# Performance work log

Hardware: AMD Instinct MI355X
Metric: run time of the kernel (lower is better)

The kernel has to match this reference:

```python
import jax, jax.numpy as jnp
import numpy as np
from jax.scipy.special import logsumexp

B, K = 256, 6144            # batch, info block length (n = 3K, rate 1/3)
NUM_ITER = 6
MU = 3                      # memory of RSC code (constraint_length 4)
NS = 1 << MU                # 8 trellis states
G0 = (1, 0, 1, 1)           # feedback polynomial '1011'
G1 = (1, 1, 0, 1)           # output polynomial  '1101'
NEG = -1e30


def _build_trellis():
    nxt = np.zeros((NS, 2), np.int32)
    par = np.zeros((NS, 2), np.int32)
    for s in range(NS):
        r = [(s >> (MU - 1 - j)) & 1 for j in range(MU)]  # r[0] newest register bit
        for u in (0, 1):
            fb = (u + sum(G0[j + 1] * r[j] for j in range(MU))) % 2
            p = (G1[0] * fb + sum(G1[j + 1] * r[j] for j in range(MU))) % 2
            nxt[s, u] = (fb << (MU - 1)) | (s >> 1)
            par[s, u] = p
    prev_s = np.zeros((NS, 2), np.int32)
    prev_u = np.zeros((NS, 2), np.int32)
    cnt = np.zeros(NS, np.int32)
    for s in range(NS):
        for u in (0, 1):
            sn = nxt[s, u]
            prev_s[sn, cnt[sn]] = s
            prev_u[sn, cnt[sn]] = u
            cnt[sn] += 1
    return nxt, par, prev_s, prev_u

_NXT, _PAR, _PREV_S, _PREV_U = _build_trellis()


def bcjr(l_sys, l_par, l_a):
    """log-MAP BCJR on the rate-1/2 RSC trellis. LLR convention log p(0)/p(1).
    l_sys, l_par, l_a: [B, K] -> posterior LLR [B, K]."""
    nxt = jnp.asarray(_NXT)
    prev_s = jnp.asarray(_PREV_S)
    prev_u = jnp.asarray(_PREV_U)
    par_sign = jnp.asarray(1.0 - 2.0 * _PAR, l_sys.dtype)  # [NS,2]
    u_sign = jnp.asarray([1.0, -1.0], l_sys.dtype)         # (1-2u)
    b = l_sys.shape[0]
    lsu = (l_sys + l_a).T                                  # [K,B]
    lp = l_par.T
    # branch metrics gamma[t, b, s, u] = 0.5*((1-2u)(Lsys+La) + (1-2p)Lpar)
    gamma = 0.5 * (lsu[:, :, None, None] * u_sign + lp[:, :, None, None] * par_sign)
    alpha0 = jnp.full((b, NS), NEG, l_sys.dtype).at[:, 0].set(0.0)  # start in state 0

    def fwd(alpha, g):
        a = logsumexp(alpha[:, prev_s] + g[:, prev_s, prev_u], axis=-1)  # [B,NS]
        a = a - jnp.max(a, axis=-1, keepdims=True)
        return a, alpha

    _, alphas = jax.lax.scan(fwd, alpha0, gamma)           # alphas[t] = alpha_t  [K,B,NS]
    beta_end = jnp.zeros((b, NS), l_sys.dtype)             # unterminated: uniform

    def bwd(beta, g):
        bn = logsumexp(g + beta[:, nxt], axis=-1)          # [B,NS]
        bn = bn - jnp.max(bn, axis=-1, keepdims=True)
        return bn, beta

    _, betas1 = jax.lax.scan(bwd, beta_end, gamma, reverse=True)  # betas1[t] = beta_{t+1}
    m = alphas[..., None] + gamma + betas1[:, :, nxt]      # [K,B,NS,2]
    l_post = logsumexp(m[..., 0], axis=-1) - logsumexp(m[..., 1], axis=-1)  # [K,B]
    return l_post.T


def turbo_decode(inputs, perm):
    llr = -inputs                 # sionna logits log p1/p0 -> internal LLR log p0/p1
    ls1 = llr[:, 0::3]            # systematic
    lp1 = llr[:, 1::3]            # parity of encoder 1
    lp2 = llr[:, 2::3]            # parity of encoder 2
    ls2 = ls1[:, perm]            # interleaved systematic for decoder 2
    inv = jnp.argsort(perm)       # deinterleave index
    le2_de = jnp.zeros_like(ls1)
    for _ in range(NUM_ITER):
        la1 = le2_de
        lpost1 = bcjr(ls1, lp1, la1)
        le1 = lpost1 - la1 - ls1                  # extrinsic of decoder 1
        la2 = le1[:, perm]
        lpost2 = bcjr(ls2, lp2, la2)
        le2_de = (lpost2 - la2 - ls2)[:, inv]     # deinterleaved extrinsic of decoder 2
    return -lpost2[:, inv]        # soft output, back to logit convention (hard_out=False)


def setup_inputs() -> dict:
    key = jax.random.key(0)
    k1, k2 = jax.random.split(key)
    inputs = jax.random.normal(k1, (B, 3 * K), dtype=jnp.float32)
    perm = jax.random.permutation(k2, K)
    return {"inputs": inputs, "perm": perm}


def reference(inputs, perm):
    return turbo_decode(inputs, perm)
```

## Files before the change

kernel.cpp:

```cpp
#include <hip/hip_runtime.h>
#include <hip/hip_fp16.h>

constexpr int B_ = 256;
constexpr int K_ = 6144;
constexpr int NITER = 6;
constexpr int L_ = 6;
constexpr int W0_ = 6;
constexpr int C_ = K_ / L_;
constexpr float LOG2E = 1.4426950408889634f;
constexpr float LN2   = 0.6931471805599453f;

static_assert(K_ % L_ == 0, "");
static_assert((L_ % 2) == 0 && (W0_ % 2) == 0, "");
static_assert(W0_ <= L_, "uniform-warmup trick requires W0 <= L");

#if __has_builtin(__builtin_amdgcn_exp2f)
#define EXP2F(x) __builtin_amdgcn_exp2f(x)
#else
#define EXP2F(x) exp2f(x)
#endif
#if __has_builtin(__builtin_amdgcn_logf)
#define LOG2F(x) __builtin_amdgcn_logf(x)
#else
#define LOG2F(x) log2f(x)
#endif
#if __has_builtin(__builtin_amdgcn_rcpf)
#define RCPF(x) __builtin_amdgcn_rcpf(x)
#else
#define RCPF(x) (1.0f / (x))
#endif

__device__ __forceinline__ float b2f(unsigned short u) {
  return __uint_as_float((unsigned)u << 16);
}
__device__ __forceinline__ unsigned short f2b(float f) {
  unsigned u = __float_as_uint(f);
  u += 0x7FFFu + ((u >> 16) & 1u);
  return (unsigned short)(u >> 16);
}
__device__ __forceinline__ float h2f_bits(unsigned short us) {
  __half_raw r; r.x = us; return __half2float(__half(r));
}
__device__ __forceinline__ unsigned short f2h_bits(float f) {
  return __half_as_ushort(__float2half(f));
}

__device__ __forceinline__ unsigned int ld_dev_u32(const unsigned int* p) {
  return __hip_atomic_load(const_cast<unsigned int*>(p), __ATOMIC_RELAXED,
                           __HIP_MEMORY_SCOPE_AGENT);
}
__device__ __forceinline__ void st_dev_u32(unsigned int* p, unsigned int v) {
  __hip_atomic_store(p, v, __ATOMIC_RELAXED, __HIP_MEMORY_SCOPE_AGENT);
}
__device__ __forceinline__ unsigned long long ld_dev_u64(
    const unsigned long long* p) {
  return __hip_atomic_load(const_cast<unsigned long long*>(p),
                           __ATOMIC_RELAXED, __HIP_MEMORY_SCOPE_AGENT);
}
__device__ __forceinline__ void st_dev_u64(unsigned long long* p,
                                           unsigned long long v) {
  __hip_atomic_store(p, v, __ATOMIC_RELAXED, __HIP_MEMORY_SCOPE_AGENT);
}

__device__ __forceinline__ void gam_lin(float gxv, float gyv, float g[4]) {
  float es = EXP2F(-fabsf(gxv));
  float ep = EXP2F(-fabsf(gyv));
  float fu0 = gxv >= 0.0f ? 1.0f : es;
  float fu1 = gxv >= 0.0f ? es : 1.0f;
  float fp0 = gyv >= 0.0f ? 1.0f : ep;
  float fp1 = gyv >= 0.0f ? ep : 1.0f;
  g[0] = fu0 * fp0; g[1] = fu0 * fp1;
  g[2] = fu1 * fp0; g[3] = fu1 * fp1;
}

__device__ __forceinline__ void step_fwd_lin(float a[8], const float g[4]) {
  float an[8];
#pragma unroll
  for (int sn = 0; sn < 8; ++sn) {
    const int u0 = ((sn >> 2) ^ (sn & 1)) & 1;
    const int p0 = ((sn >> 2) ^ ((sn >> 1) & 1)) & 1;
    an[sn] = a[(sn & 3) * 2] * g[u0 * 2 + p0]
           + a[(sn & 3) * 2 + 1] * g[(u0 ^ 1) * 2 + (p0 ^ 1)];
  }
#pragma unroll
  for (int s = 0; s < 8; ++s) a[s] = an[s];
}

__device__ __forceinline__ void step_bwd_lin(float bt[8], const float g[4]) {
  float bn[8];
#pragma unroll
  for (int s = 0; s < 8; ++s) {
    const int s0 = s & 1, s1b = (s >> 1) & 1, s2b = (s >> 2) & 1;
    const int f0 = s1b ^ s0, q = s1b ^ s2b;
    bn[s] = g[q] * bt[(f0 << 2) | (s >> 1)]
          + g[2 + (q ^ 1)] * bt[((f0 ^ 1) << 2) | (s >> 1)];
  }
#pragma unroll
  for (int s = 0; s < 8; ++s) bt[s] = bn[s];
}

__device__ __forceinline__ void renorm_lin(float a[8]) {
  float m = fmaxf(fmaxf(fmaxf(a[0], a[1]), fmaxf(a[2], a[3])),
                  fmaxf(fmaxf(a[4], a[5]), fmaxf(a[6], a[7])));
  float r = RCPF(fmaxf(m, 1e-30f));
#pragma unroll
  for (int s = 0; s < 8; ++s) a[s] = fmaf(a[s], r, 1e-32f);
}

__device__ __forceinline__ unsigned long long pack8_log8(const float a[8]) {
  unsigned int us[8];
#pragma unroll
  for (int s = 0; s < 8; ++s) {
    float l = -16.0f * LOG2F(a[s]);
    l = fminf(l, 255.0f);
    us[s] = (unsigned int)(l + 0.5f);
  }
  unsigned int x = us[0] | (us[1] << 8) | (us[2] << 16) | (us[3] << 24);
  unsigned int y = us[4] | (us[5] << 8) | (us[6] << 16) | (us[7] << 24);
  return ((unsigned long long)y << 32) | x;
}

__device__ __forceinline__ void unpack8_log8(unsigned long long v, float a[8]) {
  unsigned int vx = (unsigned int)v, vy = (unsigned int)(v >> 32);
#pragma unroll
  for (int s = 0; s < 4; ++s)
    a[s] = EXP2F(-0.0625f * (float)((vx >> (8 * s)) & 0xFFu));
#pragma unroll
  for (int s = 0; s < 4; ++s)
    a[4 + s] = EXP2F(-0.0625f * (float)((vy >> (8 * s)) & 0xFFu));
}

constexpr int NSLOT = 2 * NITER - 1;
constexpr int SLOT_U = 65 * 32;
constexpr int BARS_U = 24576;

__device__ __forceinline__ void tree_barrier(unsigned int* slotBase,
                                             unsigned int gsz) {
  __syncthreads();
  if (threadIdx.x == 0) {
    asm volatile("s_waitcnt vmcnt(0)" ::: "memory");
    const unsigned int g = blockIdx.x & 31u;
    unsigned int* cnt = slotBase + g * 32;
    unsigned int* rel = slotBase + (32 + g) * 32;
    unsigned int* root = slotBase + 64 * 32;
    unsigned int m = __hip_atomic_fetch_add(cnt, 1u, __ATOMIC_RELAXED,
                                            __HIP_MEMORY_SCOPE_AGENT);
    if (m == gsz - 1u) {
      unsigned int r = __hip_atomic_fetch_add(root, 1u, __ATOMIC_RELAXED,
                                              __HIP_MEMORY_SCOPE_AGENT);
      if (r == 31u) {
#pragma unroll
        for (int gg = 0; gg < 32; ++gg)
          st_dev_u32(slotBase + (32 + gg) * 32, 1u);
      }
    }
    while (!ld_dev_u32(rel))
      __builtin_amdgcn_s_sleep(2);
  }
  __syncthreads();
}

struct WSL {
  float* lpostT;
  __half* gx1; __half* gx2;
  unsigned short* gy1; unsigned short* gy2;
  __half* ls1; __half* ls2;
  int* inv;
  unsigned int* bars;
  unsigned long long *S1a, *S1b, *T1a, *T1b, *S2a, *S2b, *T2a, *T2b;
};

__host__ __device__ inline WSL ws_layout(char* ws) {
  const size_t KB = (size_t)K_ * B_;
  WSL w; char* p = ws;
  w.lpostT = (float*)p;            p += KB * 4;
  w.gx1    = (__half*)p;           p += KB * 2;
  w.gx2    = (__half*)p;           p += KB * 2;
  w.gy1    = (unsigned short*)p;   p += KB * 2;
  w.gy2    = (unsigned short*)p;   p += KB * 2;
  w.ls1    = (__half*)p;           p += KB * 2;
  w.ls2    = (__half*)p;           p += KB * 2;
  w.inv    = (int*)p;              p += (size_t)K_ * 4;
  w.bars   = (unsigned int*)p;     p += (size_t)BARS_U * 4;
  const size_t SB = (size_t)(C_ + 1) * B_;
  w.S1a = (unsigned long long*)p;  p += SB * 8;
  w.S1b = (unsigned long long*)p;  p += SB * 8;
  w.T1a = (unsigned long long*)p;  p += SB * 8;
  w.T1b = (unsigned long long*)p;  p += SB * 8;
  w.S2a = (unsigned long long*)p;  p += SB * 8;
  w.S2b = (unsigned long long*)p;  p += SB * 8;
  w.T2a = (unsigned long long*)p;  p += SB * 8;
  w.T2b = (unsigned long long*)p;  p += SB * 8;
  return w;
}

template <bool DEV>
__device__ __forceinline__ void half_body(
    const int c,
    const __half* __restrict__ gx,
    const unsigned short* __restrict__ gy,
    const __half* __restrict__ lsloc,
    const int* __restrict__ map,
    __half* __restrict__ gxother,
    float* __restrict__ lpost_out,
    const unsigned long long* __restrict__ Sread,
    unsigned long long* __restrict__ Swrite,
    const unsigned long long* __restrict__ Tread,
    unsigned long long* __restrict__ Twrite,
    int wmode, int mode, int wrS, bool gxc) {
  const int b = threadIdx.x;
  const int kv = c * L_;
  const int kend = kv + L_;
  const unsigned int* gxp = (const unsigned int*)gx;
  const int bh = b >> 1;
  const unsigned int hsel = (b & 1) * 16;
  const bool gdev = DEV && !gxc;

  float gvx[L_];
  unsigned short rgy[L_];
  __half hls[L_];
#pragma unroll
  for (int i = 0; i < L_; ++i) {
    size_t o2 = (size_t)(kv + i) * (B_ / 2) + bh;
    unsigned int u = gdev ? ld_dev_u32(gxp + o2) : gxp[o2];
    gvx[i] = h2f_bits((unsigned short)(u >> hsel));
    rgy[i] = gy[(size_t)(kv + i) * B_ + b];
  }
  if (mode == 0) {
#pragma unroll
    for (int i = 0; i < L_; ++i)
      hls[i] = lsloc[(size_t)(kv + i) * B_ + b];
  }
  int jmap[L_];
#pragma unroll
  for (int i = 0; i < L_; ++i) jmap[i] = map[kv + i];
  unsigned long long sraw = 0, traw = 0;
  float wfx[W0_], wbx[W0_];
  unsigned short wfy[W0_], wby[W0_];
  if (wmode == 2) {
    if (c > 0) {
      const size_t o = (size_t)c * B_ + b;
      sraw = DEV ? ld_dev_u64(Sread + o) : Sread[o];
    }
    if (c < C_ - 1) {
      const size_t o = (size_t)(c + 1) * B_ + b;
      traw = DEV ? ld_dev_u64(Tread + o) : Tread[o];
    }
  } else {
    if (c > 0) {
#pragma unroll
      for (int q = 0; q < W0_; ++q) {
        size_t o2 = (size_t)(kv - W0_ + q) * (B_ / 2) + bh;
        unsigned int u = gdev ? ld_dev_u32(gxp + o2) : gxp[o2];
        wfx[q] = h2f_bits((unsigned short)(u >> hsel));
        wfy[q] = gy[(size_t)(kv - W0_ + q) * B_ + b];
      }
    }
    if (c < C_ - 1) {
#pragma unroll
      for (int q = 0; q < W0_; ++q) {
        size_t o2 = (size_t)(kend + W0_ - 1 - q) * (B_ / 2) + bh;
        unsigned int u = gdev ? ld_dev_u32(gxp + o2) : gxp[o2];
        wbx[q] = h2f_bits((unsigned short)(u >> hsel));
        wby[q] = gy[(size_t)(kend + W0_ - 1 - q) * B_ + b];
      }
    }
  }

  float gc[L_][4];
#pragma unroll
  for (int i = 0; i < L_; ++i) gam_lin(gvx[i], b2f(rgy[i]), gc[i]);

  float a[8];
  if (c == 0) {
    a[0] = 1.0f;
#pragma unroll
    for (int s = 1; s < 8; ++s) a[s] = 0.0f;
  } else if (wmode == 0) {
    if (c == 1) {
      a[0] = 1.0f;
#pragma unroll
      for (int s = 1; s < 8; ++s) a[s] = 0.0f;
    } else {
#pragma unroll
      for (int s = 0; s < 8; ++s) a[s] = 1.0f;
    }
#pragma unroll
    for (int q = 0; q < W0_; ++q) {
      float g[4];
      gam_lin(wfx[q], b2f(wfy[q]), g);
      step_fwd_lin(a, g);
      if (q & 1) renorm_lin(a);
    }
  } else {
    unpack8_log8(sraw, a);
  }
  float a2d[L_][8];
#pragma unroll
  for (int i = 0; i < L_; ++i) {
#pragma unroll
    for (int s = 0; s < 8; ++s) a2d[i][s] = a[s];
    step_fwd_lin(a, gc[i]);
    if (i & 1) renorm_lin(a);
  }
  if (wrS) {
    unsigned long long v = pack8_log8(a);
    unsigned long long* p = Swrite + (size_t)(c + 1) * B_ + b;
    if (DEV) st_dev_u64(p, v); else *p = v;
  }

  float bt[8];
  if (c == C_ - 1) {
#pragma unroll
    for (int s = 0; s < 8; ++s) bt[s] = 1.0f;
  } else if (wmode == 0) {
#pragma unroll
    for (int s = 0; s < 8; ++s) bt[s] = 1.0f;
#pragma unroll
    for (int q = 0; q < W0_; ++q) {
      float g[4];
      gam_lin(wbx[q], b2f(wby[q]), g);
      step_bwd_lin(bt, g);
      if (q & 1) renorm_lin(bt);
    }
  } else {
    unpack8_log8(traw, bt);
  }
#pragma unroll
  for (int ii = 0; ii < L_; ++ii) {
    const int i = L_ - 1 - ii;
    const float* g = gc[i];
    float s00 = 0.0f, s01 = 0.0f, s10 = 0.0f, s11 = 0.0f;
    float bn[8];
#pragma unroll
    for (int s = 0; s < 8; ++s) {
      const int s0 = s & 1, s1b = (s >> 1) & 1, s2b = (s >> 2) & 1;
      const int f0 = s1b ^ s0, q = s1b ^ s2b;
      float b0 = bt[(f0 << 2) | (s >> 1)];
      float b1 = bt[((f0 ^ 1) << 2) | (s >> 1)];
      float m0 = a2d[i][s] * b0;
      float m1 = a2d[i][s] * b1;
      if (q == 0) { s00 += m0; s10 += m1; } else { s01 += m0; s11 += m1; }
      bn[s] = g[q] * b0 + g[2 + (q ^ 1)] * b1;
    }
    float t0 = g[0] * s00 + g[1] * s01;
    float t1 = g[3] * s10 + g[2] * s11;
    float lpost = LOG2F(fmaxf(t0, 1e-37f)) - LOG2F(fmaxf(t1, 1e-37f));
    if (mode == 0) {
      float le = lpost - gvx[i];
      unsigned short us = f2h_bits(__half2float(hls[i]) + le);
      unsigned int po = (unsigned int)__shfl_xor((int)us, 1);
      if (!(b & 1)) {
        unsigned int u = (unsigned int)us | (po << 16);
        unsigned int* p =
            (unsigned int*)gxother + ((size_t)jmap[i] * (B_ / 2) + bh);
        if (DEV) st_dev_u32(p, u); else *p = u;
      }
    } else {
      lpost_out[(size_t)jmap[i] * B_ + b] = -LN2 * lpost;
    }
#pragma unroll
    for (int s = 0; s < 8; ++s) bt[s] = bn[s];
    if (ii & 1) renorm_lin(bt);
  }
  if (wrS) {
    unsigned long long v = pack8_log8(bt);
    unsigned long long* p = Twrite + (size_t)c * B_ + b;
    if (DEV) st_dev_u64(p, v); else *p = v;
  }
}

__global__ __launch_bounds__(256, 4) void k_fused(const int* __restrict__ perm,
                                                  char* __restrict__ ws) {
  WSL w = ws_layout(ws);
  const int tid = threadIdx.x;
  const unsigned int gsz = gridDim.x >> 5;

  for (int c = blockIdx.x; c < C_; c += gridDim.x) {
#pragma unroll
    for (int r = 0; r < L_; ++r) {
      const int j = c * L_ + r;
      w.ls2[(size_t)j * B_ + tid] = w.ls1[(size_t)perm[j] * B_ + tid];
    }
  }

  int slot = 0;
  for (int it = 0; it < NITER; ++it) {
    const int pr = it & 1;
    const int wm = (it == 0) ? 0 : 2;
    const int wrS = (it != NITER - 1) ? 1 : 0;
    unsigned long long* S1r = pr ? w.S1b : w.S1a;
    unsigned long long* S1w = pr ? w.S1a : w.S1b;
    unsigned long long* T1r = pr ? w.T1b : w.T1a;
    unsigned long long* T1w = pr ? w.T1a : w.T1b;
    unsigned long long* S2r = pr ? w.S2b : w.S2a;
    unsigned long long* S2w = pr ? w.S2a : w.S2b;
    unsigned long long* T2r = pr ? w.T2b : w.T2a;
    unsigned long long* T2w = pr ? w.T2a : w.T2b;
    for (int c = blockIdx.x; c < C_; c += gridDim.x)
      half_body<true>(c, w.gx1, w.gy1, w.ls1, w.inv, w.gx2, w.lpostT,
                      S1r, S1w, T1r, T1w, wm, 0, wrS, it == 0);
    tree_barrier(w.bars + slot * SLOT_U, gsz); ++slot;
    for (int c = blockIdx.x; c < C_; c += gridDim.x)
      half_body<true>(c, w.gx2, w.gy2, w.ls2, perm, w.gx1, w.lpostT,
                      S2r, S2w, T2r, T2w, wm, (it == NITER - 1) ? 1 : 0, wrS,
                      false);
    if (it != NITER - 1) { tree_barrier(w.bars + slot * SLOT_U, gsz); ++slot; }
  }
}

__global__ __launch_bounds__(256, 4) void k_half(
    const __half* __restrict__ gx, const unsigned short* __restrict__ gy,
    const __half* __restrict__ lsloc, const int* __restrict__ map,
    __half* __restrict__ gxother, float* __restrict__ lpost_out,
    const unsigned long long* __restrict__ Sread,
    unsigned long long* __restrict__ Swrite,
    const unsigned long long* __restrict__ Tread,
    unsigned long long* __restrict__ Twrite,
    int wmode, int mode, int wrS) {
  half_body<false>(blockIdx.x, gx, gy, lsloc, map, gxother, lpost_out,
                   Sread, Swrite, Tread, Twrite, wmode, mode, wrS, true);
}

__global__ __launch_bounds__(256) void k_prep2(const __half* __restrict__ ls1,
                                               const int* __restrict__ perm,
                                               __half* __restrict__ ls2) {
  const int b = threadIdx.x;
#pragma unroll
  for (int r = 0; r < 8; ++r) {
    const int j = blockIdx.x * 8 + r;
    ls2[(size_t)j * B_ + b] = ls1[(size_t)perm[j] * B_ + b];
  }
}

__global__ __launch_bounds__(256) void k_out(const float* __restrict__ lpostT,
                                             float* __restrict__ out) {
  __shared__ float t[64][65];
  const int tid = threadIdx.x;
  const int i0 = blockIdx.x * 64, b0 = blockIdx.y * 64;
  const int tb = tid & 63, iq = tid >> 6;
  for (int ii = iq; ii < 64; ii += 4) {
    t[ii][tb] = lpostT[(size_t)(i0 + ii) * B_ + (b0 + tb)];
  }
  __syncthreads();
  const int ik = tid & 63, bq = tid >> 6;
  for (int bb = bq; bb < 64; bb += 4) {
    out[(size_t)(b0 + bb) * K_ + (i0 + ik)] = t[ik][bb];
  }
}

__global__ __launch_bounds__(256) void k_prep1(const float* __restrict__ inp,
                                               const int* __restrict__ perm,
                                               __half* __restrict__ gx1,
                                               __half* __restrict__ ls1,
                                               unsigned short* __restrict__ gy1,
                                               unsigned short* __restrict__ gy2,
                                               int* __restrict__ inv,
                                               unsigned int* __restrict__ bars) {
  __shared__ float t[3][64][65];
  const int tid = threadIdx.x;
  const int k0 = blockIdx.x * 64, b0 = blockIdx.y * 64;
  const int tk = tid & 63, tq = tid >> 6;
  for (int bb = tq; bb < 64; bb += 4) {
    size_t base = (size_t)(b0 + bb) * (3 * K_) + 3 * (size_t)(k0 + tk);
    t[0][bb][tk] = inp[base + 0];
    t[1][bb][tk] = inp[base + 1];
    t[2][bb][tk] = inp[base + 2];
  }
  __syncthreads();
  const int tb = tid & 63, kq = tid >> 6;
  for (int kk = kq; kk < 64; kk += 4) {
    size_t o = (size_t)(k0 + kk) * B_ + (b0 + tb);
    float sv = -LOG2E * t[0][tb][kk];
    float p1 = -LOG2E * t[1][tb][kk];
    float p2 = -LOG2E * t[2][tb][kk];
    ls1[o] = __float2half(sv);
    gy1[o] = f2b(p1);
    gy2[o] = f2b(p2);
    if (!(tb & 1)) {
      float sv1 = -LOG2E * t[0][tb + 1][kk];
      unsigned int u = (unsigned int)f2h_bits(sv) |
                       ((unsigned int)f2h_bits(sv1) << 16);
      ((unsigned int*)gx1)[o >> 1] = u;
    }
  }
  if (blockIdx.y == 0 && tid < 64) {
    const int j = k0 + tid;
    inv[perm[j]] = j;
  }
  if (blockIdx.y == 1 && blockIdx.x < BARS_U / 1024) {
#pragma unroll
    for (int r = 0; r < 4; ++r)
      bars[(size_t)blockIdx.x * 1024 + r * 256 + tid] = 0;
  }
}

static void launch_fallback(const int* perm, float* out, char* wsb,
                            hipStream_t stream) {
  WSL w = ws_layout(wsb);
  k_prep2<<<K_ / 8, 256, 0, stream>>>(w.ls1, perm, w.ls2);
  for (int it = 0; it < NITER; ++it) {
    const int pr = it & 1;
    const int wm = (it == 0) ? 0 : 2;
    const int wrS = (it != NITER - 1) ? 1 : 0;
    unsigned long long* S1r = pr ? w.S1b : w.S1a;
    unsigned long long* S1w = pr ? w.S1a : w.S1b;
    unsigned long long* T1r = pr ? w.T1b : w.T1a;
    unsigned long long* T1w = pr ? w.T1a : w.T1b;
    unsigned long long* S2r = pr ? w.S2b : w.S2a;
    unsigned long long* S2w = pr ? w.S2a : w.S2b;
    unsigned long long* T2r = pr ? w.T2b : w.T2a;
    unsigned long long* T2w = pr ? w.T2a : w.T2b;
    k_half<<<C_, 256, 0, stream>>>(w.gx1, w.gy1, w.ls1, w.inv, w.gx2,
                                   w.lpostT, S1r, S1w, T1r, T1w, wm, 0, wrS);
    k_half<<<C_, 256, 0, stream>>>(w.gx2, w.gy2, w.ls2, perm, w.gx1,
                                   w.lpostT, S2r, S2w, T2r, T2w, wm,
                                   (it == NITER - 1) ? 1 : 0, wrS);
  }
  k_out<<<dim3(K_ / 64, B_ / 64), 256, 0, stream>>>(w.lpostT, out);
}

extern "C" void kernel_launch(void* const* d_in, const int* in_sizes, int n_in,
                              void* d_out, int out_size, void* d_ws, size_t ws_size,
                              hipStream_t stream) {
  (void)in_sizes; (void)n_in; (void)out_size; (void)ws_size;
  const float* inp = (const float*)d_in[0];
  const int* perm = (const int*)d_in[1];
  float* out = (float*)d_out;
  char* wsb = (char*)d_ws;
  WSL w = ws_layout(wsb);

  k_prep1<<<dim3(K_ / 64, B_ / 64), 256, 0, stream>>>(
      inp, perm, w.gx1, w.ls1, w.gy1, w.gy2, w.inv, w.bars);

  static int g_mode = 0;
  static int g_grid = 0;

  if (g_mode == 0) {
    int nb = 0;
    if (hipOccupancyMaxActiveBlocksPerMultiprocessor(&nb, k_fused, 256, 0)
            != hipSuccess)
      nb = 0;
    int ncu = 0;
    hipDeviceProp_t prop;
    int dev = 0;
    (void)hipGetDevice(&dev);
    if (hipGetDeviceProperties(&prop, dev) == hipSuccess)
      ncu = prop.multiProcessorCount;
    long long g = (long long)nb * (long long)ncu;
    int grid = (g > C_) ? C_ : (int)g;
    grid &= ~31;
    if (grid >= 32) { g_mode = 1; g_grid = grid; }
    else            { g_mode = 2; }
  }

  if (g_mode == 1) {
    k_fused<<<g_grid, 256, 0, stream>>>(perm, wsb);
    k_out<<<dim3(K_ / 64, B_ / 64), 256, 0, stream>>>(w.lpostT, out);
  } else {
    launch_fallback(perm, out, wsb, stream);
  }
}
```

Measured before the change: 243.7 us.

## Pack four chunks per 1024-thread block and exchange chunk boundaries through LDS

The persistent fused kernel now runs 256 blocks of 1024 threads, each covering four consecutive trellis chunks. Boundary alpha/beta states between chunks of the same block are passed through shared memory instead of global memory. The output transpose moves into the fused kernel after a final grid barrier, and extrinsic writes are widened to 64-bit stores. The fixed grid depends on every block being co-resident (four 1024-thread blocks per CU), and the larger blocks may raise register pressure.

```diff
diff --git a/kernel.cpp b/kernel.cpp
--- a/kernel.cpp
+++ b/kernel.cpp
@@ -7,12 +7,15 @@
 constexpr int L_ = 6;
 constexpr int W0_ = 6;
 constexpr int C_ = K_ / L_;
+constexpr int CPB = 4;
+constexpr int GRID = C_ / CPB;
 constexpr float LOG2E = 1.4426950408889634f;
 constexpr float LN2   = 0.6931471805599453f;
 
 static_assert(K_ % L_ == 0, "");
 static_assert((L_ % 2) == 0 && (W0_ % 2) == 0, "");
 static_assert(W0_ <= L_, "uniform-warmup trick requires W0 <= L");
+static_assert(C_ % CPB == 0, "");
 
 #if __has_builtin(__builtin_amdgcn_exp2f)
 #define EXP2F(x) __builtin_amdgcn_exp2f(x)
@@ -52,6 +55,13 @@
 __device__ __forceinline__ void st_dev_u32(unsigned int* p, unsigned int v) {
   __hip_atomic_store(p, v, __ATOMIC_RELAXED, __HIP_MEMORY_SCOPE_AGENT);
 }
+__device__ __forceinline__ float ld_dev_f32(const float* p) {
+  return __hip_atomic_load(const_cast<float*>(p), __ATOMIC_RELAXED,
+                           __HIP_MEMORY_SCOPE_AGENT);
+}
+__device__ __forceinline__ void st_dev_f32(float* p, float v) {
+  __hip_atomic_store(p, v, __ATOMIC_RELAXED, __HIP_MEMORY_SCOPE_AGENT);
+}
 __device__ __forceinline__ unsigned long long ld_dev_u64(
     const unsigned long long* p) {
   return __hip_atomic_load(const_cast<unsigned long long*>(p),
@@ -130,9 +140,9 @@
     a[4 + s] = EXP2F(-0.0625f * (float)((vy >> (8 * s)) & 0xFFu));
 }
 
-constexpr int NSLOT = 2 * NITER - 1;
+constexpr int NSLOT = 2 * NITER;
 constexpr int SLOT_U = 65 * 32;
-constexpr int BARS_U = 24576;
+constexpr int BARS_U = 28672;
 
 __device__ __forceinline__ void tree_barrier(unsigned int* slotBase,
                                              unsigned int gsz) {
@@ -207,8 +217,9 @@
     unsigned long long* __restrict__ Swrite,
     const unsigned long long* __restrict__ Tread,
     unsigned long long* __restrict__ Twrite,
-    int wmode, int mode, int wrS, bool gxc) {
-  const int b = threadIdx.x;
+    const unsigned long long* lds_sr, unsigned long long* lds_sw,
+    const unsigned long long* lds_tr, unsigned long long* lds_tw,
+    int b, int wmode, int mode, int wrS, bool gxc) {
   const int kv = c * L_;
   const int kend = kv + L_;
   const unsigned int* gxp = (const unsigned int*)gx;
@@ -239,12 +250,18 @@
   unsigned short wfy[W0_], wby[W0_];
   if (wmode == 2) {
     if (c > 0) {
-      const size_t o = (size_t)c * B_ + b;
-      sraw = DEV ? ld_dev_u64(Sread + o) : Sread[o];
+      if (lds_sr) sraw = *lds_sr;
+      else {
+        const size_t o = (size_t)c * B_ + b;
+        sraw = DEV ? ld_dev_u64(Sread + o) : Sread[o];
+      }
     }
     if (c < C_ - 1) {
-      const size_t o = (size_t)(c + 1) * B_ + b;
-      traw = DEV ? ld_dev_u64(Tread + o) : Tread[o];
+      if (lds_tr) traw = *lds_tr;
+      else {
+        const size_t o = (size_t)(c + 1) * B_ + b;
+        traw = DEV ? ld_dev_u64(Tread + o) : Tread[o];
+      }
     }
   } else {
     if (c > 0) {
@@ -305,8 +322,11 @@
   }
   if (wrS) {
     unsigned long long v = pack8_log8(a);
-    unsigned long long* p = Swrite + (size_t)(c + 1) * B_ + b;
-    if (DEV) st_dev_u64(p, v); else *p = v;
+    if (lds_sw) *lds_sw = v;
+    else {
+      unsigned long long* p = Swrite + (size_t)(c + 1) * B_ + b;
+      if (DEV) st_dev_u64(p, v); else *p = v;
+    }
   }
 
   float bt[8];
@@ -350,14 +370,20 @@
       float le = lpost - gvx[i];
       unsigned short us = f2h_bits(__half2float(hls[i]) + le);
       unsigned int po = (unsigned int)__shfl_xor((int)us, 1);
-      if (!(b & 1)) {
-        unsigned int u = (unsigned int)us | (po << 16);
-        unsigned int* p =
-            (unsigned int*)gxother + ((size_t)jmap[i] * (B_ / 2) + bh);
-        if (DEV) st_dev_u32(p, u); else *p = u;
+      unsigned int u32v = (b & 1) ? (po | ((unsigned int)us << 16))
+                                  : ((unsigned int)us | (po << 16));
+      unsigned int uhi = (unsigned int)__shfl_xor((int)u32v, 2);
+      if ((b & 3) == 0) {
+        unsigned long long v64 =
+            (unsigned long long)u32v | ((unsigned long long)uhi << 32);
+        unsigned long long* p =
+            (unsigned long long*)gxother + ((size_t)jmap[i] * (B_ / 4) + (b >> 2));
+        if (DEV) st_dev_u64(p, v64); else *p = v64;
       }
     } else {
-      lpost_out[(size_t)jmap[i] * B_ + b] = -LN2 * lpost;
+      float v = -LN2 * lpost;
+      float* p = lpost_out + ((size_t)jmap[i] * B_ + b);
+      if (DEV) st_dev_f32(p, v); else *p = v;
     }
 #pragma unroll
     for (int s = 0; s < 8; ++s) bt[s] = bn[s];
@@ -365,28 +391,34 @@
   }
   if (wrS) {
     unsigned long long v = pack8_log8(bt);
-    unsigned long long* p = Twrite + (size_t)c * B_ + b;
-    if (DEV) st_dev_u64(p, v); else *p = v;
-  }
-}
-
-__global__ __launch_bounds__(256, 4) void k_fused(const int* __restrict__ perm,
-                                                  char* __restrict__ ws) {
+    if (lds_tw) *lds_tw = v;
+    else {
+      unsigned long long* p = Twrite + (size_t)c * B_ + b;
+      if (DEV) st_dev_u64(p, v); else *p = v;
+    }
+  }
+}
+
+__global__ __launch_bounds__(1024, 4) void k_fused(const int* __restrict__ perm,
+                                                   float* __restrict__ out,
+                                                   char* __restrict__ ws) {
   WSL w = ws_layout(ws);
+  __shared__ unsigned long long ldsST[2][2][2][3][256];
   const int tid = threadIdx.x;
+  const int q = tid >> 8;
+  const int b = tid & 255;
+  const int c = blockIdx.x * CPB + q;
   const unsigned int gsz = gridDim.x >> 5;
 
-  for (int c = blockIdx.x; c < C_; c += gridDim.x) {
-#pragma unroll
-    for (int r = 0; r < L_; ++r) {
-      const int j = c * L_ + r;
-      w.ls2[(size_t)j * B_ + tid] = w.ls1[(size_t)perm[j] * B_ + tid];
-    }
+#pragma unroll
+  for (int r = 0; r < L_; ++r) {
+    const int j = c * L_ + r;
+    w.ls2[(size_t)j * B_ + b] = w.ls1[(size_t)perm[j] * B_ + b];
   }
 
   int slot = 0;
   for (int it = 0; it < NITER; ++it) {
-    const int pr = it & 1;
+    const int pr = it & 1, pw = pr ^ 1;
     const int wm = (it == 0) ? 0 : 2;
     const int wrS = (it != NITER - 1) ? 1 : 0;
     unsigned long long* S1r = pr ? w.S1b : w.S1a;
@@ -397,15 +429,36 @@
     unsigned long long* S2w = pr ? w.S2a : w.S2b;
     unsigned long long* T2r = pr ? w.T2b : w.T2a;
     unsigned long long* T2w = pr ? w.T2a : w.T2b;
-    for (int c = blockIdx.x; c < C_; c += gridDim.x)
-      half_body<true>(c, w.gx1, w.gy1, w.ls1, w.inv, w.gx2, w.lpostT,
-                      S1r, S1w, T1r, T1w, wm, 0, wrS, it == 0);
+    half_body<true>(c, w.gx1, w.gy1, w.ls1, w.inv, w.gx2, w.lpostT,
+                    S1r, S1w, T1r, T1w,
+                    (q > 0) ? &ldsST[0][0][pr][q - 1][b] : nullptr,
+                    (q < 3) ? &ldsST[0][0][pw][q][b] : nullptr,
+                    (q < 3) ? &ldsST[1][0][pr][q][b] : nullptr,
+                    (q > 0) ? &ldsST[1][0][pw][q - 1][b] : nullptr,
+                    b, wm, 0, wrS, it == 0);
     tree_barrier(w.bars + slot * SLOT_U, gsz); ++slot;
-    for (int c = blockIdx.x; c < C_; c += gridDim.x)
-      half_body<true>(c, w.gx2, w.gy2, w.ls2, perm, w.gx1, w.lpostT,
-                      S2r, S2w, T2r, T2w, wm, (it == NITER - 1) ? 1 : 0, wrS,
-                      false);
-    if (it != NITER - 1) { tree_barrier(w.bars + slot * SLOT_U, gsz); ++slot; }
+    half_body<true>(c, w.gx2, w.gy2, w.ls2, perm, w.gx1, w.lpostT,
+                    S2r, S2w, T2r, T2w,
+                    (q > 0) ? &ldsST[0][1][pr][q - 1][b] : nullptr,
+                    (q < 3) ? &ldsST[0][1][pw][q][b] : nullptr,
+                    (q < 3) ? &ldsST[1][1][pr][q][b] : nullptr,
+                    (q > 0) ? &ldsST[1][1][pw][q - 1][b] : nullptr,
+                    b, wm, (it == NITER - 1) ? 1 : 0, wrS, false);
+    tree_barrier(w.bars + slot * SLOT_U, gsz); ++slot;
+  }
+
+  float* tt = reinterpret_cast<float*>(&ldsST[0][0][0][0][0]);
+  for (int t = blockIdx.x; t < (K_ / 64) * (B_ / 64); t += gridDim.x) {
+    const int i0 = (t >> 2) * 64;
+    const int b0 = (t & 3) * 64;
+    __syncthreads();
+    const int tb = tid & 63, iq = tid >> 6;
+    for (int ii = iq; ii < 64; ii += 16)
+      tt[ii * 65 + tb] =
+          ld_dev_f32(w.lpostT + (size_t)(i0 + ii) * B_ + (b0 + tb));
+    __syncthreads();
+    for (int bb = iq; bb < 64; bb += 16)
+      out[(size_t)(b0 + bb) * K_ + (i0 + tb)] = tt[tb * 65 + bb];
   }
 }
 
@@ -419,7 +472,9 @@
     unsigned long long* __restrict__ Twrite,
     int wmode, int mode, int wrS) {
   half_body<false>(blockIdx.x, gx, gy, lsloc, map, gxother, lpost_out,
-                   Sread, Swrite, Tread, Twrite, wmode, mode, wrS, true);
+                   Sread, Swrite, Tread, Twrite,
+                   nullptr, nullptr, nullptr, nullptr,
+                   threadIdx.x, wmode, mode, wrS, true);
 }
 
 __global__ __launch_bounds__(256) void k_prep2(const __half* __restrict__ ls1,
@@ -534,11 +589,10 @@
       inp, perm, w.gx1, w.ls1, w.gy1, w.gy2, w.inv, w.bars);
 
   static int g_mode = 0;
-  static int g_grid = 0;
 
   if (g_mode == 0) {
     int nb = 0;
-    if (hipOccupancyMaxActiveBlocksPerMultiprocessor(&nb, k_fused, 256, 0)
+    if (hipOccupancyMaxActiveBlocksPerMultiprocessor(&nb, k_fused, 1024, 0)
             != hipSuccess)
       nb = 0;
     int ncu = 0;
@@ -547,16 +601,11 @@
     (void)hipGetDevice(&dev);
     if (hipGetDeviceProperties(&prop, dev) == hipSuccess)
       ncu = prop.multiProcessorCount;
-    long long g = (long long)nb * (long long)ncu;
-    int grid = (g > C_) ? C_ : (int)g;
-    grid &= ~31;
-    if (grid >= 32) { g_mode = 1; g_grid = grid; }
-    else            { g_mode = 2; }
+    g_mode = ((long long)nb * ncu >= GRID && (GRID % 32) == 0) ? 1 : 2;
   }
 
   if (g_mode == 1) {
-    k_fused<<<g_grid, 256, 0, stream>>>(perm, wsb);
-    k_out<<<dim3(K_ / 64, B_ / 64), 256, 0, stream>>>(w.lpostT, out);
+    k_fused<<<GRID, 1024, 0, stream>>>(perm, out, wsb);
   } else {
     launch_fallback(perm, out, wsb, stream);
   }
```

Result: faster. 212.7 us (-12.7%).
